# Kernel tuning notes

Hardware: AMD Instinct MI355X
Metric: run time of the kernel (lower is better)

Reference implementation:

```python
import jax, jax.numpy as jnp
import numpy as np

B, S, D1, D2, NH, DFF, K, L = 16, 512, 512, 256, 8, 1024, 8192, 3
DK = D2 // NH
EPS_LN = 1e-5


def layer_norm(x, g, b):
    m = jnp.mean(x, axis=-1, keepdims=True)
    v = jnp.mean((x - m) ** 2, axis=-1, keepdims=True)
    return (x - m) * jax.lax.rsqrt(v + EPS_LN) * g + b


def setup_inputs() -> dict:
    key = jax.random.key(0)
    ks = jax.random.split(key, 16)
    w = lambda k, sh: (jax.random.normal(k, sh, dtype=jnp.float32) * 0.02)
    inp = {
        'x': jax.random.normal(ks[0], (B, S, D1), dtype=jnp.float32),
        'w_in': w(ks[1], (D1, D2)), 'b_in': jnp.zeros((D2,), jnp.float32),
        # per-layer stacked transformer params, leading dim = L
        'wq': w(ks[2], (L, D2, D2)), 'bq': jnp.zeros((L, D2), jnp.float32),
        'wk': w(ks[3], (L, D2, D2)), 'bk': jnp.zeros((L, D2), jnp.float32),
        'wv': w(ks[4], (L, D2, D2)), 'bv': jnp.zeros((L, D2), jnp.float32),
        'wo': w(ks[5], (L, D2, D2)), 'bo': jnp.zeros((L, D2), jnp.float32),
        'ln1_g': jnp.ones((L, D2), jnp.float32), 'ln1_b': jnp.zeros((L, D2), jnp.float32),
        'ln2_g': jnp.ones((L, D2), jnp.float32), 'ln2_b': jnp.zeros((L, D2), jnp.float32),
        'ff1_w': w(ks[6], (L, D2, DFF)), 'ff1_b': jnp.zeros((L, DFF), jnp.float32),
        'ff2_w': w(ks[7], (L, DFF, D2)), 'ff2_b': jnp.zeros((L, D2), jnp.float32),
        'pre_g': jnp.ones((D2,), jnp.float32), 'pre_b': jnp.zeros((D2,), jnp.float32),
        # codebook ~ U(-1/K, 1/K) as in torch init
        'codebook': jax.random.uniform(ks[8], (K, D2), jnp.float32, -1.0 / K, 1.0 / K),
    }
    return inp


def _encoder(x, w_in, b_in, wq, bq, wk, bk, wv, bv, wo, bo,
             ln1_g, ln1_b, ln2_g, ln2_b, ff1_w, ff1_b, ff2_w, ff2_b,
             pre_g, pre_b, codebook):
    h = x @ w_in + b_in  # [B,S,D2]
    scale = 1.0 / jnp.sqrt(jnp.float32(DK))
    for i in range(L):
        q = (h @ wq[i] + bq[i]).reshape(B, S, NH, DK)
        k = (h @ wk[i] + bk[i]).reshape(B, S, NH, DK)
        v = (h @ wv[i] + bv[i]).reshape(B, S, NH, DK)
        scores = jnp.einsum('bqhd,bkhd->bhqk', q, k) * scale
        attn = jax.nn.softmax(scores, axis=-1)  # dropout = identity (eval)
        ctx = jnp.einsum('bhqk,bkhd->bqhd', attn, v).reshape(B, S, D2)
        h = layer_norm(h + (ctx @ wo[i] + bo[i]), ln1_g[i], ln1_b[i])
        ff = jax.nn.gelu(h @ ff1_w[i] + ff1_b[i], approximate=False) @ ff2_w[i] + ff2_b[i]
        h = layer_norm(h + ff, ln2_g[i], ln2_b[i])
    h = layer_norm(h, pre_g, pre_b)

    # --- Vector quantization (L2 branch) ---
    flat = h.reshape(-1, D2)  # [N, D2], N = B*S
    dists = (jnp.sum(flat ** 2, axis=1, keepdims=True)
             + jnp.sum(codebook ** 2, axis=1)
             - 2.0 * flat @ codebook.T)  # [N, K]
    idx = jnp.argmin(dists, axis=1)  # [N]
    quant = codebook[idx].reshape(B, S, D2)  # gather == one-hot matmul
    sg = jax.lax.stop_gradient
    e_loss = jnp.mean((sg(quant) - h) ** 2)
    q_loss = jnp.mean((quant - sg(h)) ** 2)
    loss = q_loss + 0.25 * e_loss
    quant_st = h + sg(quant - h)  # straight-through
    n = jnp.float32(flat.shape[0])
    avg_probs = jnp.zeros((K,), jnp.float32).at[idx].add(1.0) / n
    perplexity = jnp.exp(-jnp.sum(avg_probs * jnp.log(avg_probs + 1e-10)))
    return quant_st, loss, perplexity, idx.reshape(B, S)


def reference(x, w_in, b_in, wq, bq, wk, bk, wv, bv, wo, bo,
              ln1_g, ln1_b, ln2_g, ln2_b, ff1_w, ff1_b, ff2_w, ff2_b,
              pre_g, pre_b, codebook):
    return _encoder(x, w_in, b_in, wq, bq, wk, bk, wv, bv, wo, bo,
                    ln1_g, ln1_b, ln2_g, ln2_b, ff1_w, ff1_b, ff2_w, ff2_b,
                    pre_g, pre_b, codebook)
```

## Files before the change

### kernel.cpp

```cpp
#include <hip/hip_runtime.h>
#include <cfloat>
#include <math.h>


#define NTOK 8192

__device__ __forceinline__ float np_pairwise256(const float* xs, int lane) {
  float r = 0.f;
  if (lane < 16) {
    const int b = lane >> 3, j = lane & 7;
    const float* p = xs + b * 128 + j;
    r = p[0];
#pragma unroll
    for (int i = 1; i < 16; i++) r += p[i * 8];
  }
  float r0 = __shfl(r, 0), r1 = __shfl(r, 1), r2 = __shfl(r, 2), r3 = __shfl(r, 3);
  float r4 = __shfl(r, 4), r5 = __shfl(r, 5), r6 = __shfl(r, 6), r7 = __shfl(r, 7);
  float s0 = ((r0 + r1) + (r2 + r3)) + ((r4 + r5) + (r6 + r7));
  float q0 = __shfl(r, 8), q1 = __shfl(r, 9), q2 = __shfl(r, 10), q3 = __shfl(r, 11);
  float q4 = __shfl(r, 12), q5 = __shfl(r, 13), q6 = __shfl(r, 14), q7 = __shfl(r, 15);
  float s1 = ((q0 + q1) + (q2 + q3)) + ((q4 + q5) + (q6 + q7));
  return s0 + s1;
}

__device__ __forceinline__ float gelu_np(float x) {
  const float SQRT2F = 1.4142135623730951f;
  float xs = x / SQRT2F;
  float e = (float)erf((double)xs);
  float t = 1.0f + e;
  return (0.5f * x) * t;
}

__device__ __forceinline__ void gemm128_core(
    const float* __restrict__ A, const float* __restrict__ Bw,
    const float* __restrict__ bias, float* __restrict__ C,
    int M, int N, int K, int act, int m0, int n0)
{
  __shared__ float As[16][132];
  __shared__ float Bs[16][132];
  const int tid = threadIdx.x;
  const int tx = tid & 15, ty = tid >> 4;
  const int ar = tid >> 1;
  const int ak = (tid & 1) * 8;
  const int brr = tid >> 5;
  const int bnn = (tid & 31) * 4;
  float accb[8][8] = {};
  const float* Ap = A + (m0 + ar) * K + ak;
  const float* Bp = Bw + brr * N + n0 + bnn;

  for (int k0 = 0; k0 < K; k0 += 16) {
    float4 a0 = *(const float4*)(Ap);
    float4 a1 = *(const float4*)(Ap + 4);
    float4 b0 = *(const float4*)(Bp);
    float4 b1 = *(const float4*)(Bp + 8 * N);
    As[ak + 0][ar] = a0.x; As[ak + 1][ar] = a0.y;
    As[ak + 2][ar] = a0.z; As[ak + 3][ar] = a0.w;
    As[ak + 4][ar] = a1.x; As[ak + 5][ar] = a1.y;
    As[ak + 6][ar] = a1.z; As[ak + 7][ar] = a1.w;
    *(float4*)&Bs[brr][bnn] = b0;
    *(float4*)&Bs[brr + 8][bnn] = b1;
    __syncthreads();
#pragma unroll
    for (int kk = 0; kk < 16; kk++) {
      float4 av0 = *(const float4*)&As[kk][ty * 8];
      float4 av1 = *(const float4*)&As[kk][ty * 8 + 4];
      float4 bv0 = *(const float4*)&Bs[kk][tx * 4];
      float4 bv1 = *(const float4*)&Bs[kk][64 + tx * 4];
      float a[8] = {av0.x, av0.y, av0.z, av0.w, av1.x, av1.y, av1.z, av1.w};
      float b[8] = {bv0.x, bv0.y, bv0.z, bv0.w, bv1.x, bv1.y, bv1.z, bv1.w};
#pragma unroll
      for (int i = 0; i < 8; i++)
#pragma unroll
        for (int j = 0; j < 8; j++) accb[i][j] = fmaf(a[i], b[j], accb[i][j]);
    }
    __syncthreads();
    Ap += 16;
    Bp += 16 * N;
  }
  float4 bbl = make_float4(0.f, 0.f, 0.f, 0.f);
  float4 bbh = make_float4(0.f, 0.f, 0.f, 0.f);
  if (bias) {
    bbl = *(const float4*)&bias[n0 + tx * 4];
    bbh = *(const float4*)&bias[n0 + 64 + tx * 4];
  }
#pragma unroll
  for (int i = 0; i < 8; i++) {
    const int m = m0 + ty * 8 + i;
    float4 lo, hi;
    lo.x = accb[i][0] + bbl.x; lo.y = accb[i][1] + bbl.y;
    lo.z = accb[i][2] + bbl.z; lo.w = accb[i][3] + bbl.w;
    hi.x = accb[i][4] + bbh.x; hi.y = accb[i][5] + bbh.y;
    hi.z = accb[i][6] + bbh.z; hi.w = accb[i][7] + bbh.w;
    if (act == 1) {
      lo.x = gelu_np(lo.x); lo.y = gelu_np(lo.y);
      lo.z = gelu_np(lo.z); lo.w = gelu_np(lo.w);
      hi.x = gelu_np(hi.x); hi.y = gelu_np(hi.y);
      hi.z = gelu_np(hi.z); hi.w = gelu_np(hi.w);
    }
    *(float4*)&C[m * N + n0 + tx * 4] = lo;
    *(float4*)&C[m * N + n0 + 64 + tx * 4] = hi;
  }
}

__global__ __launch_bounds__(256) void qkv_kernel(
    const float* __restrict__ h,
    const float* __restrict__ wq, const float* __restrict__ bq,
    const float* __restrict__ wk, const float* __restrict__ bk,
    const float* __restrict__ wv, const float* __restrict__ bv,
    float* __restrict__ Q, float* __restrict__ K, float* __restrict__ V)
{
  const int sel = blockIdx.y >> 1;
  const int n0 = (blockIdx.y & 1) * 128;
  const float* W = (sel == 0) ? wq : (sel == 1) ? wk : wv;
  const float* bb = (sel == 0) ? bq : (sel == 1) ? bk : bv;
  float* C = (sel == 0) ? Q : (sel == 1) ? K : V;
  gemm128_core(h, W, bb, C, NTOK, 256, 256, 0, blockIdx.x * 128, n0);
}

__global__ __launch_bounds__(256) void gemm128_kernel(
    const float* __restrict__ A, const float* __restrict__ B,
    const float* __restrict__ bias, float* __restrict__ C,
    int M, int N, int K, int act)
{
  gemm128_core(A, B, bias, C, M, N, K, act, blockIdx.x * 128, blockIdx.y * 128);
}

__global__ __launch_bounds__(256) void gemm64_kernel(
    const float* __restrict__ A, const float* __restrict__ B,
    const float* __restrict__ bias, float* __restrict__ C,
    int M, int N, int K, int act)
{
  __shared__ float As[2][16][68];
  __shared__ float Bs[2][16][68];
  const int tid = threadIdx.x;
  const int tx = tid & 15, ty = tid >> 4;
  const int m0 = blockIdx.x * 64, n0 = blockIdx.y * 64;
  const int ar = tid >> 2;
  const int ak = (tid & 3) * 4;
  const int br = tid >> 4;
  const int bn = (tid & 15) * 4;
  const float* Ap = A + (m0 + ar) * K + ak;
  const float* Bp = B + br * N + n0 + bn;
  float acc[4][4] = {};
  float accb[4][4] = {};
  const int nk = K >> 4;

  float4 aR = *(const float4*)(Ap);
  float4 bR = *(const float4*)(Bp);
  As[0][ak + 0][ar] = aR.x; As[0][ak + 1][ar] = aR.y;
  As[0][ak + 2][ar] = aR.z; As[0][ak + 3][ar] = aR.w;
  *(float4*)&Bs[0][br][bn] = bR;

  for (int t = 0; t < nk; t++) {
    const int p = t & 1;
    __syncthreads();
    if (t + 1 < nk) {
      aR = *(const float4*)(Ap + (t + 1) * 16);
      bR = *(const float4*)(Bp + (t + 1) * 16 * N);
    }
#pragma unroll
    for (int kk = 0; kk < 16; kk++) {
      float4 av = *(const float4*)&As[p][kk][ty * 4];
      float4 bv = *(const float4*)&Bs[p][kk][tx * 4];
      float a[4] = {av.x, av.y, av.z, av.w};
      float b[4] = {bv.x, bv.y, bv.z, bv.w};
#pragma unroll
      for (int i = 0; i < 4; i++)
#pragma unroll
        for (int j = 0; j < 4; j++) accb[i][j] = fmaf(a[i], b[j], accb[i][j]);
    }
    if (((((t + 1) << 4) % 384) == 0) || (t + 1 == nk)) {
#pragma unroll
      for (int i = 0; i < 4; i++)
#pragma unroll
        for (int j = 0; j < 4; j++) { acc[i][j] += accb[i][j]; accb[i][j] = 0.f; }
    }
    if (t + 1 < nk) {
      const int q = p ^ 1;
      As[q][ak + 0][ar] = aR.x; As[q][ak + 1][ar] = aR.y;
      As[q][ak + 2][ar] = aR.z; As[q][ak + 3][ar] = aR.w;
      *(float4*)&Bs[q][br][bn] = bR;
    }
  }
  float4 bb4 = make_float4(0.f, 0.f, 0.f, 0.f);
  if (bias) bb4 = *(const float4*)&bias[n0 + tx * 4];
#pragma unroll
  for (int i = 0; i < 4; i++) {
    float4 o;
    o.x = acc[i][0] + bb4.x;
    o.y = acc[i][1] + bb4.y;
    o.z = acc[i][2] + bb4.z;
    o.w = acc[i][3] + bb4.w;
    if (act == 1) {
      o.x = gelu_np(o.x); o.y = gelu_np(o.y);
      o.z = gelu_np(o.z); o.w = gelu_np(o.w);
    }
    *(float4*)&C[(m0 + ty * 4 + i) * N + n0 + tx * 4] = o;
  }
}

__global__ __launch_bounds__(256) void attn_kernel(
    const float* __restrict__ Q, const float* __restrict__ Kb,
    const float* __restrict__ Vb, float* __restrict__ ctx)
{
  __shared__ float Kc[128][32];
  __shared__ float Vc[128][32];
  const int bh = blockIdx.x;
  const int b = bh >> 3, h = bh & 7;
  const int s = blockIdx.y * 256 + threadIdx.x;
  const int base = (b * 512) * 256 + h * 32;

  float q[32];
  const float* qrow = Q + base + s * 256;
#pragma unroll
  for (int d = 0; d < 32; d += 4) {
    float4 t = *(const float4*)(qrow + d);
    q[d] = t.x; q[d + 1] = t.y; q[d + 2] = t.z; q[d + 3] = t.w;
  }
  float l = 0.f;
  float acc[32] = {};
  const float scale = 0.17677669529663687f;

  for (int kc = 0; kc < 4; kc++) {
#pragma unroll
    for (int r = 0; r < 4; r++) {
      int ff = threadIdx.x + r * 256;
      int j = ff >> 3;
      int d0 = (ff & 7) * 4;
      int tok = kc * 128 + j;
      *(float4*)&Kc[j][d0] = *(const float4*)(Kb + base + tok * 256 + d0);
      *(float4*)&Vc[j][d0] = *(const float4*)(Vb + base + tok * 256 + d0);
    }
    __syncthreads();
#pragma unroll 2
    for (int j = 0; j < 128; j += 2) {
      const float* k0r = &Kc[j][0];
      const float* k1r = &Kc[j + 1][0];
      float a0 = 0.f, a1 = 0.f, a2 = 0.f, a3 = 0.f;
      float b0 = 0.f, b1 = 0.f, b2 = 0.f, b3 = 0.f;
#pragma unroll
      for (int d = 0; d < 32; d += 4) {
        a0 = fmaf(q[d], k0r[d], a0);
        a1 = fmaf(q[d + 1], k0r[d + 1], a1);
        a2 = fmaf(q[d + 2], k0r[d + 2], a2);
        a3 = fmaf(q[d + 3], k0r[d + 3], a3);
        b0 = fmaf(q[d], k1r[d], b0);
        b1 = fmaf(q[d + 1], k1r[d + 1], b1);
        b2 = fmaf(q[d + 2], k1r[d + 2], b2);
        b3 = fmaf(q[d + 3], k1r[d + 3], b3);
      }
      float p0 = expf(((a0 + a1) + (a2 + a3)) * scale);
      float p1 = expf(((b0 + b1) + (b2 + b3)) * scale);
      l += p0;
      l += p1;
      const float* v0r = &Vc[j][0];
      const float* v1r = &Vc[j + 1][0];
#pragma unroll
      for (int d = 0; d < 32; d++)
        acc[d] = fmaf(p1, v1r[d], fmaf(p0, v0r[d], acc[d]));
    }
    __syncthreads();
  }
  float inv = 1.f / l;
  float* crow = ctx + base + s * 256;
#pragma unroll
  for (int d = 0; d < 32; d += 4) {
    float4 o;
    o.x = acc[d] * inv; o.y = acc[d + 1] * inv;
    o.z = acc[d + 2] * inv; o.w = acc[d + 3] * inv;
    *(float4*)(crow + d) = o;
  }
}

__global__ __launch_bounds__(256) void ln_kernel(
    const float* __restrict__ X, const float* __restrict__ R,
    const float* __restrict__ g, const float* __restrict__ bt,
    float* __restrict__ Y, int hasR)
{
  __shared__ float rows[4][256];
  const int w = threadIdx.x >> 6, lane = threadIdx.x & 63;
  const int row = blockIdx.x * 4 + w;
  float4 xv = *(const float4*)(X + row * 256 + lane * 4);
  if (hasR) {
    float4 rv = *(const float4*)(R + row * 256 + lane * 4);
    xv.x += rv.x; xv.y += rv.y; xv.z += rv.z; xv.w += rv.w;
  }
  *(float4*)&rows[w][lane * 4] = xv;
  __syncthreads();
  float sum = np_pairwise256(rows[w], lane);
  float mean = sum * (1.0f / 256.0f);
  float dx = xv.x - mean, dy = xv.y - mean, dz = xv.z - mean, dw = xv.w - mean;
  __syncthreads();
  float4 sq; sq.x = dx * dx; sq.y = dy * dy; sq.z = dz * dz; sq.w = dw * dw;
  *(float4*)&rows[w][lane * 4] = sq;
  __syncthreads();
  float vsum = np_pairwise256(rows[w], lane);
  float var = vsum * (1.0f / 256.0f);
  float inv = 1.0f / sqrtf(var + 1e-5f);
  float4 gv = *(const float4*)(g + lane * 4);
  float4 bv = *(const float4*)(bt + lane * 4);
  float4 o;
  o.x = ((dx * inv) * gv.x) + bv.x;
  o.y = ((dy * inv) * gv.y) + bv.y;
  o.z = ((dz * inv) * gv.z) + bv.z;
  o.w = ((dw * inv) * gv.w) + bv.w;
  *(float4*)(Y + row * 256 + lane * 4) = o;
}

__global__ __launch_bounds__(256) void atok_kernel(
    const float* __restrict__ HN, float* __restrict__ Atok)
{
  __shared__ float rows[4][256];
  const int w = threadIdx.x >> 6, lane = threadIdx.x & 63;
  const int row = blockIdx.x * 4 + w;
  float4 v = *(const float4*)&HN[row * 256 + lane * 4];
  float4 sq; sq.x = v.x * v.x; sq.y = v.y * v.y; sq.z = v.z * v.z; sq.w = v.w * v.w;
  *(float4*)&rows[w][lane * 4] = sq;
  __syncthreads();
  float sum = np_pairwise256(rows[w], lane);
  if (lane == 0) Atok[row] = sum;
}

__global__ __launch_bounds__(256) void vq_partial_kernel(
    const float* __restrict__ H, const float* __restrict__ CB,
    const float* __restrict__ Atok, float* __restrict__ partV,
    int* __restrict__ partI)
{
  __shared__ float As[16][132];
  __shared__ float Bs[16][132];
  const int tid = threadIdx.x;
  const int tx = tid & 15, ty = tid >> 4;
  const int m0 = blockIdx.x * 128;
  const int cg0 = blockIdx.y * 512;
  const int ar = tid >> 1;
  const int ak = (tid & 1) * 8;
  float At[8];
#pragma unroll
  for (int i = 0; i < 8; i++) At[i] = Atok[m0 + ty * 8 + i];
  float bestV[8];
  int bestI[8];
#pragma unroll
  for (int i = 0; i < 8; i++) { bestV[i] = FLT_MAX; bestI[i] = 0; }

  for (int ct = 0; ct < 4; ct++) {
    const int c0 = cg0 + ct * 128;
    float acc[8][8] = {};
    const float* Ap = H + (m0 + ar) * 256 + ak;
    const float* Bp = CB + (c0 + ar) * 256 + ak;
    for (int k0 = 0; k0 < 256; k0 += 16) {
      float4 a0 = *(const float4*)(Ap);
      float4 a1 = *(const float4*)(Ap + 4);
      float4 c0v = *(const float4*)(Bp);
      float4 c1v = *(const float4*)(Bp + 4);
      As[ak + 0][ar] = a0.x; As[ak + 1][ar] = a0.y;
      As[ak + 2][ar] = a0.z; As[ak + 3][ar] = a0.w;
      As[ak + 4][ar] = a1.x; As[ak + 5][ar] = a1.y;
      As[ak + 6][ar] = a1.z; As[ak + 7][ar] = a1.w;
      Bs[ak + 0][ar] = c0v.x; Bs[ak + 1][ar] = c0v.y;
      Bs[ak + 2][ar] = c0v.z; Bs[ak + 3][ar] = c0v.w;
      Bs[ak + 4][ar] = c1v.x; Bs[ak + 5][ar] = c1v.y;
      Bs[ak + 6][ar] = c1v.z; Bs[ak + 7][ar] = c1v.w;
      __syncthreads();
#pragma unroll
      for (int kk = 0; kk < 16; kk++) {
        float4 av0 = *(const float4*)&As[kk][ty * 8];
        float4 av1 = *(const float4*)&As[kk][ty * 8 + 4];
        float4 bv0 = *(const float4*)&Bs[kk][tx * 4];
        float4 bv1 = *(const float4*)&Bs[kk][64 + tx * 4];
        float a[8] = {av0.x, av0.y, av0.z, av0.w, av1.x, av1.y, av1.z, av1.w};
        float b[8] = {bv0.x, bv0.y, bv0.z, bv0.w, bv1.x, bv1.y, bv1.z, bv1.w};
#pragma unroll
        for (int i = 0; i < 8; i++)
#pragma unroll
          for (int j = 0; j < 8; j++) acc[i][j] = fmaf(a[i], b[j], acc[i][j]);
      }
      __syncthreads();
      Ap += 16;
      Bp += 16;
    }
#pragma unroll
    for (int i = 0; i < 8; i++) {
#pragma unroll
      for (int j = 0; j < 8; j++) {
        int code = c0 + ((j < 4) ? (tx * 4 + j) : (64 + tx * 4 + (j - 4)));
        float v = At[i] - 2.0f * acc[i][j];
        if (v < bestV[i]) { bestV[i] = v; bestI[i] = code; }
      }
    }
  }
#pragma unroll
  for (int i = 0; i < 8; i++) {
    float v = bestV[i];
    int ii = bestI[i];
#pragma unroll
    for (int off = 1; off < 16; off <<= 1) {
      float ov = __shfl_xor(v, off);
      int oi = __shfl_xor(ii, off);
      if (ov < v || (ov == v && oi < ii)) { v = ov; ii = oi; }
    }
    if (tx == 0) {
      int token = m0 + ty * 8 + i;
      partV[token * 16 + blockIdx.y] = v;
      partI[token * 16 + blockIdx.y] = ii;
    }
  }
}

__global__ __launch_bounds__(256) void vq_final_kernel(
    const float* __restrict__ partV, const int* __restrict__ partI,
    const float* __restrict__ HN, const float* __restrict__ CB,
    float* __restrict__ outQuant, float* __restrict__ outIdxF,
    int* __restrict__ idxInt, int* __restrict__ counts,
    float* __restrict__ lossAcc)
{
  const int w = threadIdx.x >> 6, lane = threadIdx.x & 63;
  const int t = blockIdx.x * 4 + w;
  float v = (lane < 16) ? partV[t * 16 + lane] : FLT_MAX;
  int i = (lane < 16) ? partI[t * 16 + lane] : 0x7fffffff;
#pragma unroll
  for (int off = 8; off; off >>= 1) {
    float ov = __shfl_xor(v, off);
    int oi = __shfl_xor(i, off);
    if (ov < v || (ov == v && oi < i)) { v = ov; i = oi; }
  }
  int idx = __shfl(i, 0);
  const float* c = CB + idx * 256;
  const float* hh = HN + t * 256;
  float4 cv = *(const float4*)(c + lane * 4);
  float4 hv = *(const float4*)(hh + lane * 4);
  *(float4*)(outQuant + t * 256 + lane * 4) = cv;
  float ex = cv.x - hv.x, ey = cv.y - hv.y, ez = cv.z - hv.z, ew = cv.w - hv.w;
  float se = ex * ex + ey * ey + ez * ez + ew * ew;
#pragma unroll
  for (int off = 32; off; off >>= 1) se += __shfl_xor(se, off);
  if (lane == 0) {
    outIdxF[t] = (float)idx;
    idxInt[t] = idx;
    atomicAdd(&counts[idx], 1);
    atomicAdd(lossAcc, se);
  }
}

__global__ __launch_bounds__(256) void vq_stats_kernel(
    const int* __restrict__ counts, const float* __restrict__ lossAcc,
    float* __restrict__ out)
{
  float ent = 0.f;
  for (int k = threadIdx.x; k < 8192; k += 256) {
    float p = (float)counts[k] * (1.0f / 8192.0f);
    ent += p * logf(p + 1e-10f);
  }
#pragma unroll
  for (int off = 32; off; off >>= 1) ent += __shfl_xor(ent, off);
  __shared__ float ws4[4];
  const int w = threadIdx.x >> 6, lane = threadIdx.x & 63;
  if (lane == 0) ws4[w] = ent;
  __syncthreads();
  if (threadIdx.x == 0) {
    float e = ws4[0] + ws4[1] + ws4[2] + ws4[3];
    out[2097152] = 1.25f * lossAcc[0] * (1.0f / 2097152.0f);
    out[2097153] = expf(-e);
  }
}

__global__ void zero_kernel(int* __restrict__ counts, float* __restrict__ lossAcc) {
  int i = blockIdx.x * 256 + threadIdx.x;
  if (i < 8192) counts[i] = 0;
  if (i == 0) lossAcc[0] = 0.f;
}

extern "C" void kernel_launch(void* const* d_in, const int* in_sizes, int n_in,
                              void* d_out, int out_size, void* d_ws, size_t ws_size,
                              hipStream_t stream) {
  const float* x = (const float*)d_in[0];
  const float* w_in = (const float*)d_in[1];
  const float* b_in = (const float*)d_in[2];
  const float* wq = (const float*)d_in[3];
  const float* bq = (const float*)d_in[4];
  const float* wk = (const float*)d_in[5];
  const float* bk = (const float*)d_in[6];
  const float* wv = (const float*)d_in[7];
  const float* bv = (const float*)d_in[8];
  const float* wo = (const float*)d_in[9];
  const float* bo = (const float*)d_in[10];
  const float* ln1g = (const float*)d_in[11];
  const float* ln1b = (const float*)d_in[12];
  const float* ln2g = (const float*)d_in[13];
  const float* ln2b = (const float*)d_in[14];
  const float* ff1w = (const float*)d_in[15];
  const float* ff1b = (const float*)d_in[16];
  const float* ff2w = (const float*)d_in[17];
  const float* ff2b = (const float*)d_in[18];
  const float* preg = (const float*)d_in[19];
  const float* preb = (const float*)d_in[20];
  const float* cb = (const float*)d_in[21];
  float* out = (float*)d_out;

  if (ws_size < (51ull << 20)) return;
  char* ws = (char*)d_ws;
  float* h = (float*)(ws + 0);
  float* Qb = (float*)(ws + (8ull << 20));
  float* Kb2 = (float*)(ws + (16ull << 20));
  float* Vb = (float*)(ws + (24ull << 20));
  float* Cx = (float*)(ws + (32ull << 20));
  float* Ob = Qb;
  float* F1 = Qb;
  float* F2 = (float*)(ws + (40ull << 20));
  float* HN = F2;
  float* Atok = (float*)(ws + (48ull << 20));
  float* partV = (float*)(ws + (49ull << 20));
  int* partI = (int*)(ws + (49ull << 20) + (512ull << 10));
  int* idxInt = (int*)(ws + (50ull << 20));
  int* counts = (int*)(ws + (50ull << 20) + (64ull << 10));
  float* lossAcc = (float*)(ws + (50ull << 20) + (128ull << 10));

  zero_kernel<<<32, 256, 0, stream>>>(counts, lossAcc);

  gemm64_kernel<<<dim3(128, 4), 256, 0, stream>>>(x, w_in, b_in, h, NTOK, 256, 512, 0);

  for (int i = 0; i < 3; i++) {
    qkv_kernel<<<dim3(64, 6), 256, 0, stream>>>(
        h, wq + i * 65536, bq + i * 256, wk + i * 65536, bk + i * 256,
        wv + i * 65536, bv + i * 256, Qb, Kb2, Vb);
    attn_kernel<<<dim3(128, 2), 256, 0, stream>>>(Qb, Kb2, Vb, Cx);
    gemm64_kernel<<<dim3(128, 4), 256, 0, stream>>>(Cx, wo + i * 65536, bo + i * 256, Ob, NTOK, 256, 256, 0);
    ln_kernel<<<2048, 256, 0, stream>>>(h, Ob, ln1g + i * 256, ln1b + i * 256, h, 1);
    gemm128_kernel<<<dim3(64, 8), 256, 0, stream>>>(h, ff1w + i * 262144, ff1b + i * 1024, F1, NTOK, 1024, 256, 1);
    gemm64_kernel<<<dim3(128, 4), 256, 0, stream>>>(F1, ff2w + i * 262144, ff2b + i * 256, F2, NTOK, 256, 1024, 0);
    ln_kernel<<<2048, 256, 0, stream>>>(h, F2, ln2g + i * 256, ln2b + i * 256, h, 1);
  }
  ln_kernel<<<2048, 256, 0, stream>>>(h, nullptr, preg, preb, HN, 0);

  atok_kernel<<<2048, 256, 0, stream>>>(HN, Atok);
  vq_partial_kernel<<<dim3(64, 16), 256, 0, stream>>>(HN, cb, Atok, partV, partI);
  vq_final_kernel<<<2048, 256, 0, stream>>>(partV, partI, HN, cb,
                                            out, out + 2097154, idxInt, counts, lossAcc);
  vq_stats_kernel<<<1, 256, 0, stream>>>(counts, lossAcc, out);
}
```

Measured before the change: 1.598 ms.

## Double-buffer GEMM tiles, retile attention into query blocks, fuse norm-squared into LN

The 128-wide GEMM core and the VQ distance kernel now use double-buffered shared-memory tiles: the next K-slice is loaded into registers while the current slice is computed, leaving one barrier per step. The VQ kernel also flattens its codebook-tile loop into a single pipelined loop. Attention is rewritten so each block handles 64 queries and streams 32-key tiles, storing probabilities in shared memory with a 2D thread tiling, and the launch grows to four times as many blocks. The separate row squared-norm kernel is folded into the final layer-norm, removing one launch and one read of the normalized activations. The cost is roughly double the shared memory in the GEMMs and more barriers per key tile in attention.

After: 1.708 ms. 6.9% more time.

```diff
diff --git a/kernel.cpp b/kernel.cpp
--- a/kernel.cpp
+++ b/kernel.cpp
@@ -36,8 +36,8 @@
     const float* __restrict__ bias, float* __restrict__ C,
     int M, int N, int K, int act, int m0, int n0)
 {
-  __shared__ float As[16][132];
-  __shared__ float Bs[16][132];
+  __shared__ float As[2][16][132];
+  __shared__ float Bs[2][16][132];
   const int tid = threadIdx.x;
   const int tx = tid & 15, ty = tid >> 4;
   const int ar = tid >> 1;
@@ -47,25 +47,34 @@
   float accb[8][8] = {};
   const float* Ap = A + (m0 + ar) * K + ak;
   const float* Bp = Bw + brr * N + n0 + bnn;
-
-  for (int k0 = 0; k0 < K; k0 += 16) {
-    float4 a0 = *(const float4*)(Ap);
-    float4 a1 = *(const float4*)(Ap + 4);
-    float4 b0 = *(const float4*)(Bp);
-    float4 b1 = *(const float4*)(Bp + 8 * N);
-    As[ak + 0][ar] = a0.x; As[ak + 1][ar] = a0.y;
-    As[ak + 2][ar] = a0.z; As[ak + 3][ar] = a0.w;
-    As[ak + 4][ar] = a1.x; As[ak + 5][ar] = a1.y;
-    As[ak + 6][ar] = a1.z; As[ak + 7][ar] = a1.w;
-    *(float4*)&Bs[brr][bnn] = b0;
-    *(float4*)&Bs[brr + 8][bnn] = b1;
-    __syncthreads();
+  const int nk = K >> 4;
+
+  float4 a0 = *(const float4*)(Ap);
+  float4 a1 = *(const float4*)(Ap + 4);
+  float4 b0 = *(const float4*)(Bp);
+  float4 b1 = *(const float4*)(Bp + 8 * N);
+  As[0][ak + 0][ar] = a0.x; As[0][ak + 1][ar] = a0.y;
+  As[0][ak + 2][ar] = a0.z; As[0][ak + 3][ar] = a0.w;
+  As[0][ak + 4][ar] = a1.x; As[0][ak + 5][ar] = a1.y;
+  As[0][ak + 6][ar] = a1.z; As[0][ak + 7][ar] = a1.w;
+  *(float4*)&Bs[0][brr][bnn] = b0;
+  *(float4*)&Bs[0][brr + 8][bnn] = b1;
+  __syncthreads();
+
+  for (int t = 0; t < nk; t++) {
+    const int p = t & 1;
+    if (t + 1 < nk) {
+      a0 = *(const float4*)(Ap + (t + 1) * 16);
+      a1 = *(const float4*)(Ap + (t + 1) * 16 + 4);
+      b0 = *(const float4*)(Bp + (t + 1) * 16 * N);
+      b1 = *(const float4*)(Bp + ((t + 1) * 16 + 8) * N);
+    }
 #pragma unroll
     for (int kk = 0; kk < 16; kk++) {
-      float4 av0 = *(const float4*)&As[kk][ty * 8];
-      float4 av1 = *(const float4*)&As[kk][ty * 8 + 4];
-      float4 bv0 = *(const float4*)&Bs[kk][tx * 4];
-      float4 bv1 = *(const float4*)&Bs[kk][64 + tx * 4];
+      float4 av0 = *(const float4*)&As[p][kk][ty * 8];
+      float4 av1 = *(const float4*)&As[p][kk][ty * 8 + 4];
+      float4 bv0 = *(const float4*)&Bs[p][kk][tx * 4];
+      float4 bv1 = *(const float4*)&Bs[p][kk][64 + tx * 4];
       float a[8] = {av0.x, av0.y, av0.z, av0.w, av1.x, av1.y, av1.z, av1.w};
       float b[8] = {bv0.x, bv0.y, bv0.z, bv0.w, bv1.x, bv1.y, bv1.z, bv1.w};
 #pragma unroll
@@ -73,9 +82,16 @@
 #pragma unroll
         for (int j = 0; j < 8; j++) accb[i][j] = fmaf(a[i], b[j], accb[i][j]);
     }
-    __syncthreads();
-    Ap += 16;
-    Bp += 16 * N;
+    if (t + 1 < nk) {
+      const int q = p ^ 1;
+      As[q][ak + 0][ar] = a0.x; As[q][ak + 1][ar] = a0.y;
+      As[q][ak + 2][ar] = a0.z; As[q][ak + 3][ar] = a0.w;
+      As[q][ak + 4][ar] = a1.x; As[q][ak + 5][ar] = a1.y;
+      As[q][ak + 6][ar] = a1.z; As[q][ak + 7][ar] = a1.w;
+      *(float4*)&Bs[q][brr][bnn] = b0;
+      *(float4*)&Bs[q][brr + 8][bnn] = b1;
+    }
+    __syncthreads();
   }
   float4 bbl = make_float4(0.f, 0.f, 0.f, 0.f);
   float4 bbh = make_float4(0.f, 0.f, 0.f, 0.f);
@@ -203,79 +219,100 @@
     const float* __restrict__ Q, const float* __restrict__ Kb,
     const float* __restrict__ Vb, float* __restrict__ ctx)
 {
-  __shared__ float Kc[128][32];
-  __shared__ float Vc[128][32];
-  const int bh = blockIdx.x;
-  const int b = bh >> 3, h = bh & 7;
-  const int s = blockIdx.y * 256 + threadIdx.x;
+  __shared__ float Qs[64][36];
+  __shared__ float Ks[32][36];
+  __shared__ float Vs[32][36];
+  __shared__ float Ps[64][33];
+  __shared__ float l_lds[64];
+  const int tid = threadIdx.x;
+  const int b = blockIdx.x >> 3, h = blockIdx.x & 7;
+  const int q0 = blockIdx.y * 64;
   const int base = (b * 512) * 256 + h * 32;
-
-  float q[32];
-  const float* qrow = Q + base + s * 256;
-#pragma unroll
-  for (int d = 0; d < 32; d += 4) {
-    float4 t = *(const float4*)(qrow + d);
-    q[d] = t.x; q[d + 1] = t.y; q[d + 2] = t.z; q[d + 3] = t.w;
-  }
-  float l = 0.f;
-  float acc[32] = {};
   const float scale = 0.17677669529663687f;
 
-  for (int kc = 0; kc < 4; kc++) {
-#pragma unroll
-    for (int r = 0; r < 4; r++) {
-      int ff = threadIdx.x + r * 256;
-      int j = ff >> 3;
-      int d0 = (ff & 7) * 4;
-      int tok = kc * 128 + j;
-      *(float4*)&Kc[j][d0] = *(const float4*)(Kb + base + tok * 256 + d0);
-      *(float4*)&Vc[j][d0] = *(const float4*)(Vb + base + tok * 256 + d0);
-    }
-    __syncthreads();
-#pragma unroll 2
-    for (int j = 0; j < 128; j += 2) {
-      const float* k0r = &Kc[j][0];
-      const float* k1r = &Kc[j + 1][0];
-      float a0 = 0.f, a1 = 0.f, a2 = 0.f, a3 = 0.f;
-      float b0 = 0.f, b1 = 0.f, b2 = 0.f, b3 = 0.f;
-#pragma unroll
-      for (int d = 0; d < 32; d += 4) {
-        a0 = fmaf(q[d], k0r[d], a0);
-        a1 = fmaf(q[d + 1], k0r[d + 1], a1);
-        a2 = fmaf(q[d + 2], k0r[d + 2], a2);
-        a3 = fmaf(q[d + 3], k0r[d + 3], a3);
-        b0 = fmaf(q[d], k1r[d], b0);
-        b1 = fmaf(q[d + 1], k1r[d + 1], b1);
-        b2 = fmaf(q[d + 2], k1r[d + 2], b2);
-        b3 = fmaf(q[d + 3], k1r[d + 3], b3);
+  {
+    int i0 = tid * 2;
+    int r = i0 >> 3, c = i0 & 7;
+    *(float4*)&Qs[r][c * 4] = *(const float4*)(Q + base + (q0 + r) * 256 + c * 4);
+    int i1 = i0 + 1;
+    r = i1 >> 3; c = i1 & 7;
+    *(float4*)&Qs[r][c * 4] = *(const float4*)(Q + base + (q0 + r) * 256 + c * 4);
+  }
+  if (tid < 64) l_lds[tid] = 0.f;
+
+  const int tx = tid & 15, ty = tid >> 4;
+  const int tx2 = tid & 7, ty2 = tid >> 3;
+  float acc[2][4] = {};
+
+  for (int kc = 0; kc < 16; kc++) {
+    __syncthreads();
+    {
+      int r = tid >> 3, c = tid & 7;
+      int tok = kc * 32 + r;
+      *(float4*)&Ks[r][c * 4] = *(const float4*)(Kb + base + tok * 256 + c * 4);
+      *(float4*)&Vs[r][c * 4] = *(const float4*)(Vb + base + tok * 256 + c * 4);
+    }
+    __syncthreads();
+    float s0[4] = {}, s1[4] = {};
+#pragma unroll
+    for (int d = 0; d < 32; d += 4) {
+      float4 k0 = *(const float4*)&Ks[tx][d];
+      float4 k1 = *(const float4*)&Ks[tx + 16][d];
+#pragma unroll
+      for (int i = 0; i < 4; i++) {
+        float4 qv = *(const float4*)&Qs[ty * 4 + i][d];
+        s0[i] = fmaf(qv.w, k0.w, fmaf(qv.z, k0.z, fmaf(qv.y, k0.y, fmaf(qv.x, k0.x, s0[i]))));
+        s1[i] = fmaf(qv.w, k1.w, fmaf(qv.z, k1.z, fmaf(qv.y, k1.y, fmaf(qv.x, k1.x, s1[i]))));
       }
-      float p0 = expf(((a0 + a1) + (a2 + a3)) * scale);
-      float p1 = expf(((b0 + b1) + (b2 + b3)) * scale);
-      l += p0;
-      l += p1;
-      const float* v0r = &Vc[j][0];
-      const float* v1r = &Vc[j + 1][0];
-#pragma unroll
-      for (int d = 0; d < 32; d++)
-        acc[d] = fmaf(p1, v1r[d], fmaf(p0, v0r[d], acc[d]));
-    }
-    __syncthreads();
-  }
-  float inv = 1.f / l;
-  float* crow = ctx + base + s * 256;
-#pragma unroll
-  for (int d = 0; d < 32; d += 4) {
+    }
+    float rs[4];
+#pragma unroll
+    for (int i = 0; i < 4; i++) {
+      float p0 = expf(s0[i] * scale);
+      float p1 = expf(s1[i] * scale);
+      Ps[ty * 4 + i][tx] = p0;
+      Ps[ty * 4 + i][tx + 16] = p1;
+      rs[i] = p0 + p1;
+    }
+#pragma unroll
+    for (int off = 1; off < 16; off <<= 1)
+#pragma unroll
+      for (int i = 0; i < 4; i++) rs[i] += __shfl_xor(rs[i], off);
+    if (tx == 0) {
+#pragma unroll
+      for (int i = 0; i < 4; i++) l_lds[ty * 4 + i] += rs[i];
+    }
+    __syncthreads();
+#pragma unroll 4
+    for (int k = 0; k < 32; k++) {
+      float4 vv = *(const float4*)&Vs[k][tx2 * 4];
+      float pa = Ps[ty2 * 2][k];
+      float pb = Ps[ty2 * 2 + 1][k];
+      acc[0][0] = fmaf(pa, vv.x, acc[0][0]);
+      acc[0][1] = fmaf(pa, vv.y, acc[0][1]);
+      acc[0][2] = fmaf(pa, vv.z, acc[0][2]);
+      acc[0][3] = fmaf(pa, vv.w, acc[0][3]);
+      acc[1][0] = fmaf(pb, vv.x, acc[1][0]);
+      acc[1][1] = fmaf(pb, vv.y, acc[1][1]);
+      acc[1][2] = fmaf(pb, vv.z, acc[1][2]);
+      acc[1][3] = fmaf(pb, vv.w, acc[1][3]);
+    }
+  }
+  __syncthreads();
+#pragma unroll
+  for (int i = 0; i < 2; i++) {
+    float inv = 1.f / l_lds[ty2 * 2 + i];
     float4 o;
-    o.x = acc[d] * inv; o.y = acc[d + 1] * inv;
-    o.z = acc[d + 2] * inv; o.w = acc[d + 3] * inv;
-    *(float4*)(crow + d) = o;
+    o.x = acc[i][0] * inv; o.y = acc[i][1] * inv;
+    o.z = acc[i][2] * inv; o.w = acc[i][3] * inv;
+    *(float4*)(ctx + base + (q0 + ty2 * 2 + i) * 256 + tx2 * 4) = o;
   }
 }
 
 __global__ __launch_bounds__(256) void ln_kernel(
     const float* __restrict__ X, const float* __restrict__ R,
     const float* __restrict__ g, const float* __restrict__ bt,
-    float* __restrict__ Y, int hasR)
+    float* __restrict__ Y, int hasR, float* __restrict__ Atok)
 {
   __shared__ float rows[4][256];
   const int w = threadIdx.x >> 6, lane = threadIdx.x & 63;
@@ -305,20 +342,15 @@
   o.z = ((dz * inv) * gv.z) + bv.z;
   o.w = ((dw * inv) * gv.w) + bv.w;
   *(float4*)(Y + row * 256 + lane * 4) = o;
-}
-
-__global__ __launch_bounds__(256) void atok_kernel(
-    const float* __restrict__ HN, float* __restrict__ Atok)
-{
-  __shared__ float rows[4][256];
-  const int w = threadIdx.x >> 6, lane = threadIdx.x & 63;
-  const int row = blockIdx.x * 4 + w;
-  float4 v = *(const float4*)&HN[row * 256 + lane * 4];
-  float4 sq; sq.x = v.x * v.x; sq.y = v.y * v.y; sq.z = v.z * v.z; sq.w = v.w * v.w;
-  *(float4*)&rows[w][lane * 4] = sq;
-  __syncthreads();
-  float sum = np_pairwise256(rows[w], lane);
-  if (lane == 0) Atok[row] = sum;
+  if (Atok) {
+    float4 s2; s2.x = o.x * o.x; s2.y = o.y * o.y;
+    s2.z = o.z * o.z; s2.w = o.w * o.w;
+    __syncthreads();
+    *(float4*)&rows[w][lane * 4] = s2;
+    __syncthreads();
+    float asum = np_pairwise256(rows[w], lane);
+    if (lane == 0) Atok[row] = asum;
+  }
 }
 
 __global__ __launch_bounds__(256) void vq_partial_kernel(
@@ -326,8 +358,8 @@
     const float* __restrict__ Atok, float* __restrict__ partV,
     int* __restrict__ partI)
 {
-  __shared__ float As[16][132];
-  __shared__ float Bs[16][132];
+  __shared__ float As[2][16][132];
+  __shared__ float Bs[2][16][132];
   const int tid = threadIdx.x;
   const int tx = tid & 15, ty = tid >> 4;
   const int m0 = blockIdx.x * 128;
@@ -341,52 +373,74 @@
   int bestI[8];
 #pragma unroll
   for (int i = 0; i < 8; i++) { bestV[i] = FLT_MAX; bestI[i] = 0; }
-
-  for (int ct = 0; ct < 4; ct++) {
-    const int c0 = cg0 + ct * 128;
-    float acc[8][8] = {};
-    const float* Ap = H + (m0 + ar) * 256 + ak;
-    const float* Bp = CB + (c0 + ar) * 256 + ak;
-    for (int k0 = 0; k0 < 256; k0 += 16) {
-      float4 a0 = *(const float4*)(Ap);
-      float4 a1 = *(const float4*)(Ap + 4);
-      float4 c0v = *(const float4*)(Bp);
-      float4 c1v = *(const float4*)(Bp + 4);
-      As[ak + 0][ar] = a0.x; As[ak + 1][ar] = a0.y;
-      As[ak + 2][ar] = a0.z; As[ak + 3][ar] = a0.w;
-      As[ak + 4][ar] = a1.x; As[ak + 5][ar] = a1.y;
-      As[ak + 6][ar] = a1.z; As[ak + 7][ar] = a1.w;
-      Bs[ak + 0][ar] = c0v.x; Bs[ak + 1][ar] = c0v.y;
-      Bs[ak + 2][ar] = c0v.z; Bs[ak + 3][ar] = c0v.w;
-      Bs[ak + 4][ar] = c1v.x; Bs[ak + 5][ar] = c1v.y;
-      Bs[ak + 6][ar] = c1v.z; Bs[ak + 7][ar] = c1v.w;
-      __syncthreads();
-#pragma unroll
-      for (int kk = 0; kk < 16; kk++) {
-        float4 av0 = *(const float4*)&As[kk][ty * 8];
-        float4 av1 = *(const float4*)&As[kk][ty * 8 + 4];
-        float4 bv0 = *(const float4*)&Bs[kk][tx * 4];
-        float4 bv1 = *(const float4*)&Bs[kk][64 + tx * 4];
-        float a[8] = {av0.x, av0.y, av0.z, av0.w, av1.x, av1.y, av1.z, av1.w};
-        float b[8] = {bv0.x, bv0.y, bv0.z, bv0.w, bv1.x, bv1.y, bv1.z, bv1.w};
-#pragma unroll
-        for (int i = 0; i < 8; i++)
-#pragma unroll
-          for (int j = 0; j < 8; j++) acc[i][j] = fmaf(a[i], b[j], acc[i][j]);
+  float acc[8][8] = {};
+
+  const float* Ab = H + (m0 + ar) * 256 + ak;
+  const float* Bb = CB + (cg0 + ar) * 256 + ak;
+
+  float4 a0 = *(const float4*)(Ab);
+  float4 a1 = *(const float4*)(Ab + 4);
+  float4 b0 = *(const float4*)(Bb);
+  float4 b1 = *(const float4*)(Bb + 4);
+  As[0][ak + 0][ar] = a0.x; As[0][ak + 1][ar] = a0.y;
+  As[0][ak + 2][ar] = a0.z; As[0][ak + 3][ar] = a0.w;
+  As[0][ak + 4][ar] = a1.x; As[0][ak + 5][ar] = a1.y;
+  As[0][ak + 6][ar] = a1.z; As[0][ak + 7][ar] = a1.w;
+  Bs[0][ak + 0][ar] = b0.x; Bs[0][ak + 1][ar] = b0.y;
+  Bs[0][ak + 2][ar] = b0.z; Bs[0][ak + 3][ar] = b0.w;
+  Bs[0][ak + 4][ar] = b1.x; Bs[0][ak + 5][ar] = b1.y;
+  Bs[0][ak + 6][ar] = b1.z; Bs[0][ak + 7][ar] = b1.w;
+  __syncthreads();
+
+  for (int s = 0; s < 64; s++) {
+    const int p = s & 1;
+    if (s < 63) {
+      const int s1 = s + 1;
+      const int k1 = (s1 & 15) << 4;
+      const float* Bp = Bb + (s1 >> 4) * (128 * 256) + k1;
+      a0 = *(const float4*)(Ab + k1);
+      a1 = *(const float4*)(Ab + k1 + 4);
+      b0 = *(const float4*)(Bp);
+      b1 = *(const float4*)(Bp + 4);
+    }
+#pragma unroll
+    for (int kk = 0; kk < 16; kk++) {
+      float4 av0 = *(const float4*)&As[p][kk][ty * 8];
+      float4 av1 = *(const float4*)&As[p][kk][ty * 8 + 4];
+      float4 bv0 = *(const float4*)&Bs[p][kk][tx * 4];
+      float4 bv1 = *(const float4*)&Bs[p][kk][64 + tx * 4];
+      float a[8] = {av0.x, av0.y, av0.z, av0.w, av1.x, av1.y, av1.z, av1.w};
+      float b[8] = {bv0.x, bv0.y, bv0.z, bv0.w, bv1.x, bv1.y, bv1.z, bv1.w};
+#pragma unroll
+      for (int i = 0; i < 8; i++)
+#pragma unroll
+        for (int j = 0; j < 8; j++) acc[i][j] = fmaf(a[i], b[j], acc[i][j]);
+    }
+    if ((s & 15) == 15) {
+      const int c0 = cg0 + (s >> 4) * 128;
+#pragma unroll
+      for (int i = 0; i < 8; i++) {
+#pragma unroll
+        for (int j = 0; j < 8; j++) {
+          int code = c0 + ((j < 4) ? (tx * 4 + j) : (64 + tx * 4 + (j - 4)));
+          float v = At[i] - 2.0f * acc[i][j];
+          if (v < bestV[i]) { bestV[i] = v; bestI[i] = code; }
+          acc[i][j] = 0.f;
+        }
       }
-      __syncthreads();
-      Ap += 16;
-      Bp += 16;
-    }
-#pragma unroll
-    for (int i = 0; i < 8; i++) {
-#pragma unroll
-      for (int j = 0; j < 8; j++) {
-        int code = c0 + ((j < 4) ? (tx * 4 + j) : (64 + tx * 4 + (j - 4)));
-        float v = At[i] - 2.0f * acc[i][j];
-        if (v < bestV[i]) { bestV[i] = v; bestI[i] = code; }
-      }
-    }
+    }
+    if (s < 63) {
+      const int q = p ^ 1;
+      As[q][ak + 0][ar] = a0.x; As[q][ak + 1][ar] = a0.y;
+      As[q][ak + 2][ar] = a0.z; As[q][ak + 3][ar] = a0.w;
+      As[q][ak + 4][ar] = a1.x; As[q][ak + 5][ar] = a1.y;
+      As[q][ak + 6][ar] = a1.z; As[q][ak + 7][ar] = a1.w;
+      Bs[q][ak + 0][ar] = b0.x; Bs[q][ak + 1][ar] = b0.y;
+      Bs[q][ak + 2][ar] = b0.z; Bs[q][ak + 3][ar] = b0.w;
+      Bs[q][ak + 4][ar] = b1.x; Bs[q][ak + 5][ar] = b1.y;
+      Bs[q][ak + 6][ar] = b1.z; Bs[q][ak + 7][ar] = b1.w;
+    }
+    __syncthreads();
   }
 #pragma unroll
   for (int i = 0; i < 8; i++) {
@@ -522,16 +576,15 @@
     qkv_kernel<<<dim3(64, 6), 256, 0, stream>>>(
         h, wq + i * 65536, bq + i * 256, wk + i * 65536, bk + i * 256,
         wv + i * 65536, bv + i * 256, Qb, Kb2, Vb);
-    attn_kernel<<<dim3(128, 2), 256, 0, stream>>>(Qb, Kb2, Vb, Cx);
+    attn_kernel<<<dim3(128, 8), 256, 0, stream>>>(Qb, Kb2, Vb, Cx);
     gemm64_kernel<<<dim3(128, 4), 256, 0, stream>>>(Cx, wo + i * 65536, bo + i * 256, Ob, NTOK, 256, 256, 0);
-    ln_kernel<<<2048, 256, 0, stream>>>(h, Ob, ln1g + i * 256, ln1b + i * 256, h, 1);
+    ln_kernel<<<2048, 256, 0, stream>>>(h, Ob, ln1g + i * 256, ln1b + i * 256, h, 1, nullptr);
     gemm128_kernel<<<dim3(64, 8), 256, 0, stream>>>(h, ff1w + i * 262144, ff1b + i * 1024, F1, NTOK, 1024, 256, 1);
     gemm64_kernel<<<dim3(128, 4), 256, 0, stream>>>(F1, ff2w + i * 262144, ff2b + i * 256, F2, NTOK, 256, 1024, 0);
-    ln_kernel<<<2048, 256, 0, stream>>>(h, F2, ln2g + i * 256, ln2b + i * 256, h, 1);
-  }
-  ln_kernel<<<2048, 256, 0, stream>>>(h, nullptr, preg, preb, HN, 0);
-
-  atok_kernel<<<2048, 256, 0, stream>>>(HN, Atok);
+    ln_kernel<<<2048, 256, 0, stream>>>(h, F2, ln2g + i * 256, ln2b + i * 256, h, 1, nullptr);
+  }
+  ln_kernel<<<2048, 256, 0, stream>>>(h, nullptr, preg, preb, HN, 0, Atok);
+
   vq_partial_kernel<<<dim3(64, 16), 256, 0, stream>>>(HN, cb, Atok, partV, partI);
   vq_final_kernel<<<2048, 256, 0, stream>>>(partV, partI, HN, cb,
                                             out, out + 2097154, idxInt, counts, lossAcc);
```
